# Kernel optimization log

Hardware: AMD Instinct MI355X
Metric: run time of the kernel (lower is better)

The kernel has to match this reference:

```python
import jax, jax.numpy as jnp
import numpy as np

B, S, HID = 2, 2048, 2048
H, HKV, D = 16, 4, 128        # num_heads, num_kv_heads, head_dim
G = H // HKV                   # GQA group size
CLIP = 8.0                     # clip_qkv
THETA = 10000.0                # rope_theta_within_seq
N_SEQS = 8                     # max_num_sequences


def setup_inputs() -> dict:
    key = jax.random.key(0)
    ks = jax.random.split(key, 6)
    hidden_states = jax.random.normal(ks[0], (B, S, HID), dtype=jnp.float32)
    within_seq_position_ids = jnp.broadcast_to(jnp.arange(S, dtype=jnp.int64), (B, S))
    global_position_ids = jnp.broadcast_to(jnp.arange(S, dtype=jnp.int64), (B, S))
    sequence_ids = jnp.sort(jax.random.randint(ks[1], (B, S), 0, N_SEQS, dtype=jnp.int64), axis=-1)
    scale = 0.02
    Wq = jax.random.normal(ks[2], (H * D, HID), dtype=jnp.float32) * scale
    Wk = jax.random.normal(ks[3], (HKV * D, HID), dtype=jnp.float32) * scale
    Wv = jax.random.normal(ks[4], (HKV * D, HID), dtype=jnp.float32) * scale
    Wo = jax.random.normal(ks[5], (HID, H * D), dtype=jnp.float32) * scale
    return {"hidden_states": hidden_states,
            "within_seq_position_ids": within_seq_position_ids,
            "global_position_ids": global_position_ids,
            "sequence_ids": sequence_ids,
            "Wq": Wq, "Wk": Wk, "Wv": Wv, "Wo": Wo}


def _rotate_half(x):
    x1, x2 = jnp.split(x, 2, axis=-1)
    return jnp.concatenate((-x2, x1), axis=-1)


def _rope_cos_sin(position_ids, dtype):
    # inv_freq: [D/2]
    inv_freq = THETA ** (-(jnp.arange(0, D, 2, dtype=jnp.float32) / D))
    angles = position_ids.astype(jnp.float32)[..., None] * inv_freq  # [B,S,D/2]
    angles = jnp.concatenate((angles, angles), axis=-1)              # [B,S,D]
    # unsqueeze head dim -> [B,S,1,D]
    return jnp.cos(angles)[:, :, None, :].astype(dtype), jnp.sin(angles)[:, :, None, :].astype(dtype)


def reference(hidden_states, within_seq_position_ids, global_position_ids, sequence_ids, Wq, Wk, Wv, Wo):
    b, s, _ = hidden_states.shape
    q = (hidden_states @ Wq.T).reshape(b, s, H, D)
    k = (hidden_states @ Wk.T).reshape(b, s, HKV, D)
    v = (hidden_states @ Wv.T).reshape(b, s, HKV, D)
    # clip_qkv
    q = jnp.clip(q, -CLIP, CLIP)
    k = jnp.clip(k, -CLIP, CLIP)
    v = jnp.clip(v, -CLIP, CLIP)
    # RoPE (within_seq layer -> within_seq_position_ids)
    cos, sin = _rope_cos_sin(within_seq_position_ids, q.dtype)
    q = q * cos + _rotate_half(q) * sin
    k = k * cos + _rotate_half(k) * sin
    # GQA: group queries by kv head instead of materializing repeat_kv
    q = q.transpose(0, 2, 1, 3).reshape(b, HKV, G, s, D)  # [B,HKV,G,S,D]
    k = k.transpose(0, 2, 1, 3)                            # [B,HKV,S,D]
    v = v.transpose(0, 2, 1, 3)
    scores = jnp.einsum('bhgqd,bhkd->bhgqk', q, k) / jnp.sqrt(jnp.asarray(D, q.dtype))
    # block-diagonal (same sequence) causal mask
    qi = jnp.arange(s)
    causal = qi[:, None] >= qi[None, :]                    # [S,S]
    same_seq = sequence_ids[:, :, None] == sequence_ids[:, None, :]  # [B,S,S]
    mask = (causal[None] & same_seq)[:, None, None, :, :]  # [B,1,1,S,S]
    scores = jnp.where(mask, scores, jnp.finfo(scores.dtype).min)
    attn = jax.nn.softmax(scores, axis=-1)
    out = jnp.einsum('bhgqk,bhkd->bhgqd', attn, v)         # [B,HKV,G,S,D]
    out = out.reshape(b, H, s, D).transpose(0, 2, 1, 3).reshape(b, s, H * D)
    return out @ Wo.T
```

## Files before the change

### kernel.cpp

```cpp
#include <hip/hip_runtime.h>
#include <hip/hip_bf16.h>

typedef __hip_bfloat16 bf16;
typedef __attribute__((ext_vector_type(8))) short bf16x8;
typedef __attribute__((ext_vector_type(4))) float f32x4;

#define MFMA_BF16(a, b, c) __builtin_amdgcn_mfma_f32_16x16x32_bf16((a), (b), (c), 0, 0, 0)

#define B_   2
#define S_   2048
#define HID_ 2048
#define H_   16
#define HKV_ 4
#define D_   128

#define GLOAD_LDS(gptr, lptr) \
  __builtin_amdgcn_global_load_lds((const __attribute__((address_space(1))) void*)(gptr), \
                                   (__attribute__((address_space(3))) void*)(lptr), 16, 0, 0)

template <int N>
__device__ __forceinline__ void vmw() {
  if constexpr (N == 0)      asm volatile("s_waitcnt vmcnt(0)" ::: "memory");
  else if constexpr (N == 3) asm volatile("s_waitcnt vmcnt(3)" ::: "memory");
  else                       asm volatile("s_waitcnt vmcnt(4)" ::: "memory");
}

__device__ __forceinline__ void blk_barrier() {
  __builtin_amdgcn_sched_barrier(0);
  __builtin_amdgcn_s_barrier();
  __builtin_amdgcn_sched_barrier(0);
}

__global__ void cvt_f32_bf16(const float* __restrict__ src, bf16* __restrict__ dst, int n) {
  int i = (blockIdx.x * 256 + threadIdx.x) * 4;
  if (i >= n) return;
  float4 v = *reinterpret_cast<const float4*>(src + i);
  alignas(8) bf16 t[4];
  t[0] = __float2bfloat16(v.x);
  t[1] = __float2bfloat16(v.y);
  t[2] = __float2bfloat16(v.z);
  t[3] = __float2bfloat16(v.w);
  *reinterpret_cast<short4*>(dst + i) = *reinterpret_cast<const short4*>(t);
}

__global__ void seq_start(const int* __restrict__ seq, int* __restrict__ sstart) {
  int t = blockIdx.x * 256 + threadIdx.x;
  int b = t >> 11, s = t & (S_ - 1);
  const int* sb = seq + b * S_;
  int sid = sb[s];
  int lo = 0, hi = s;
  while (lo < hi) {
    int mid = (lo + hi) >> 1;
    if (sb[mid] < sid) lo = mid + 1; else hi = mid;
  }
  sstart[t] = lo;
}

template <int BM, int OUT_BF16>
__global__ __launch_bounds__(512, 2) void gemm8p(const bf16* __restrict__ A,
                                                 const bf16* __restrict__ Bw,
                                                 void* __restrict__ Cout,
                                                 int M, int N, int K) {
  constexpr int BN = 256;
  constexpr int MR = BM / 32;
  constexpr int LA = BM / 128;
  constexpr int VCHK = (BM == 256) ? 4 : 3;

  __shared__ bf16 As[2][2][BM * 32];
  __shared__ bf16 Bs[2][2][BN * 32];

  const int tid  = threadIdx.x;
  const int lane = tid & 63;
  const int w    = tid >> 6;
  const int wr   = w >> 2;
  const int wc   = w & 3;
  const int ln15 = lane & 15, g = lane >> 4;

  const int nwg = gridDim.x;
  int bid = blockIdx.x;
  bid = (bid & 7) * (nwg >> 3) + (bid >> 3);
  const int nbn = N / BN;
  const int m0 = (bid / nbn) * BM;
  const int n0 = (bid % nbn) * BN;

  f32x4 acc[MR][4] = {};

  auto stageA = [&](int db, int kh, int t) {
    int kc = t * 64 + kh * 32;
#pragma unroll
    for (int r = 0; r < LA; r++) {
      int sIdx = r * 512 + tid;
      int row = sIdx >> 2;
      int ss = (sIdx & 3) ^ ((row >> 1) & 3);
      GLOAD_LDS(A + (size_t)(m0 + row) * K + kc + ss * 8, &As[db][kh][(r * 512 + w * 64) * 8]);
    }
  };
  auto stageB = [&](int db, int kh, int t) {
    int kc = t * 64 + kh * 32;
#pragma unroll
    for (int r = 0; r < 2; r++) {
      int sIdx = r * 512 + tid;
      int row = sIdx >> 2;
      int ss = (sIdx & 3) ^ ((row >> 1) & 3);
      GLOAD_LDS(Bw + (size_t)(n0 + row) * K + kc + ss * 8, &Bs[db][kh][(r * 512 + w * 64) * 8]);
    }
  };
  auto rdA = [&](bf16x8 (&af)[4], int db, int kh, int mb) {
#pragma unroll
    for (int m = 0; m < 4; m++) {
      int row = wr * (BM / 2) + (mb + m) * 16 + ln15;
      af[m] = *reinterpret_cast<const bf16x8*>(&As[db][kh][row * 32 + ((g ^ ((row >> 1) & 3)) << 3)]);
    }
  };
  auto rdB = [&](bf16x8 (&bfr)[4], int db, int kh) {
#pragma unroll
    for (int n = 0; n < 4; n++) {
      int row = wc * 64 + n * 16 + ln15;
      bfr[n] = *reinterpret_cast<const bf16x8*>(&Bs[db][kh][row * 32 + ((g ^ ((row >> 1) & 3)) << 3)]);
    }
  };

  bf16x8 af[4], bfr[4];
  auto MF = [&](int mb) {
    __builtin_amdgcn_s_setprio(1);
#pragma unroll
    for (int m = 0; m < 4; m++)
#pragma unroll
      for (int n = 0; n < 4; n++)
        acc[mb + m][n] = MFMA_BF16(af[m], bfr[n], acc[mb + m][n]);
    __builtin_amdgcn_s_setprio(0);
  };

  const int NT = K >> 6;

  stageA(0, 0, 0); stageB(0, 0, 0);
  stageA(0, 1, 0); stageB(0, 1, 0);
  stageA(1, 0, 1); stageB(1, 0, 1);
  vmw<VCHK>();
  blk_barrier();

  for (int T = 0; T < NT; ++T) {
    const int db = T & 1, dn = db ^ 1;
    const bool tail = (T >= NT - 3);

    if constexpr (BM == 256) {
      rdA(af, db, 0, 0); rdB(bfr, db, 0);
      if (T + 1 < NT) stageA(dn, 1, T + 1);
      blk_barrier(); MF(0); blk_barrier();
      rdA(af, db, 0, 4);
      if (T + 1 < NT) stageB(dn, 1, T + 1);
      if (tail) vmw<0>(); else vmw<4>();
      blk_barrier(); MF(4); blk_barrier();
      rdA(af, db, 1, 0); rdB(bfr, db, 1);
      if (T + 2 < NT) stageA(db, 0, T + 2);
      blk_barrier(); MF(0); blk_barrier();
      rdA(af, db, 1, 4);
      if (T + 2 < NT) stageB(db, 0, T + 2);
      if (tail) vmw<0>(); else vmw<4>();
      blk_barrier(); MF(4); blk_barrier();
    } else {
      rdA(af, db, 0, 0); rdB(bfr, db, 0);
      if (T + 1 < NT) { stageA(dn, 1, T + 1); stageB(dn, 1, T + 1); }
      if (tail) vmw<0>(); else vmw<3>();
      blk_barrier(); MF(0); blk_barrier();
      rdA(af, db, 1, 0); rdB(bfr, db, 1);
      if (T + 2 < NT) { stageA(db, 0, T + 2); stageB(db, 0, T + 2); }
      if (tail) vmw<0>(); else vmw<3>();
      blk_barrier(); MF(0); blk_barrier();
    }
  }

#pragma unroll
  for (int m = 0; m < MR; m++)
#pragma unroll
    for (int n = 0; n < 4; n++)
#pragma unroll
      for (int r = 0; r < 4; r++) {
        int row = m0 + wr * (BM / 2) + m * 16 + g * 4 + r;
        int col = n0 + wc * 64 + n * 16 + ln15;
        if constexpr (OUT_BF16) {
          ((bf16*)Cout)[(size_t)row * N + col] = __float2bfloat16(acc[m][n][r]);
        } else {
          ((float*)Cout)[(size_t)row * N + col] = acc[m][n][r];
        }
      }
}

__global__ __launch_bounds__(256) void qkv_post(const bf16* __restrict__ QKV,
                                                const int* __restrict__ wpos,
                                                bf16* __restrict__ Qs,
                                                bf16* __restrict__ Ks,
                                                bf16* __restrict__ Vt) {
  const int row = blockIdx.x;
  const int b = row >> 11, s = row & (S_ - 1);
  const int t = threadIdx.x;
  const bf16* R = QKV + (size_t)row * 3072;
  const float pos = (float)wpos[row];
  const float kln = 0.14391156831212787f;
  const float qscale = 0.08838834764831845f;

  for (int p = t; p < 1024; p += 256) {
    int h = p >> 6, i = p & 63;
    float ang = pos * expf(-(float)i * kln);
    float sn, cs;
    sincosf(ang, &sn, &cs);
    float x1 = __bfloat162float(R[h * 128 + i]);
    float x2 = __bfloat162float(R[h * 128 + 64 + i]);
    x1 = fminf(fmaxf(x1, -8.f), 8.f);
    x2 = fminf(fmaxf(x2, -8.f), 8.f);
    float y1 = (x1 * cs - x2 * sn) * qscale;
    float y2 = (x2 * cs + x1 * sn) * qscale;
    size_t qb = ((size_t)(b * H_ + h) * S_ + s) * D_;
    Qs[qb + i]      = __float2bfloat16(y1);
    Qs[qb + 64 + i] = __float2bfloat16(y2);
  }
  {
    int kh = t >> 6, i = t & 63;
    float ang = pos * expf(-(float)i * kln);
    float sn, cs;
    sincosf(ang, &sn, &cs);
    float x1 = __bfloat162float(R[2048 + kh * 128 + i]);
    float x2 = __bfloat162float(R[2048 + kh * 128 + 64 + i]);
    x1 = fminf(fmaxf(x1, -8.f), 8.f);
    x2 = fminf(fmaxf(x2, -8.f), 8.f);
    float y1 = x1 * cs - x2 * sn;
    float y2 = x2 * cs + x1 * sn;
    size_t kb = ((size_t)(b * HKV_ + kh) * S_ + s) * D_;
    Ks[kb + i]      = __float2bfloat16(y1);
    Ks[kb + 64 + i] = __float2bfloat16(y2);
  }
  for (int e = t; e < 512; e += 256) {
    int kh = e >> 7, d = e & 127;
    float x = __bfloat162float(R[2560 + e]);
    x = fminf(fmaxf(x, -8.f), 8.f);
    Vt[((size_t)(b * HKV_ + kh) * D_ + d) * S_ + s] = __float2bfloat16(x);
  }
}

__global__ __launch_bounds__(256) void attn_fwd(const bf16* __restrict__ Qs,
                                                const bf16* __restrict__ Ks,
                                                const bf16* __restrict__ Vt,
                                                const int* __restrict__ sstart,
                                                bf16* __restrict__ att) {
  __shared__ bf16 Kl[2][32 * 128];
  __shared__ bf16 Vl[2][128 * 32];
  __shared__ bf16 Plds[4][16 * 32];

  const int tid = threadIdx.x;
  const int lane = tid & 63, w = tid >> 6;
  const int ln15 = lane & 15, g = lane >> 4;

  const int wg = ((blockIdx.x & 7) << 7) | (blockIdx.x >> 3);
  const int qt  = wg & 127;
  const int kvh = (wg >> 7) & 3;
  const int b   = wg >> 9;
  const int h   = kvh * 4 + w;
  const int q0  = qt * 16;
  const int qi  = q0 + ln15;

  const bf16* Qrow = Qs + ((size_t)(b * H_ + h) * S_ + qi) * D_;
  bf16x8 qf[4];
#pragma unroll
  for (int c = 0; c < 4; c++)
    qf[c] = *reinterpret_cast<const bf16x8*>(Qrow + c * 32 + g * 8);

  const int sQ = sstart[b * S_ + qi];
  const int kstart = __builtin_amdgcn_readfirstlane(__shfl(sQ, 0));
  const int kend = q0 + 15;

  const bf16* Kb = Ks + (size_t)(b * HKV_ + kvh) * S_ * D_;
  const bf16* Vb = Vt + (size_t)(b * HKV_ + kvh) * D_ * S_;

  auto stage = [&](int buf, int kb) {
#pragma unroll
    for (int p = 0; p < 2; p++) {
      int slot = p * 256 + tid;
      int row = slot >> 4;
      int cs = (slot & 15) ^ (row & 15);
      int gr = min(kb + row, S_ - 1);
      GLOAD_LDS(Kb + (size_t)gr * D_ + cs * 8, &Kl[buf][(p * 256 + w * 64) * 8]);
    }
#pragma unroll
    for (int p = 0; p < 2; p++) {
      int slot = p * 256 + tid;
      int d = slot >> 2, c = slot & 3;
      int cs = c ^ (d & 3);
      int gcol = min(kb + cs * 8, S_ - 8);
      GLOAD_LDS(Vb + (size_t)d * S_ + gcol, &Vl[buf][(p * 256 + w * 64) * 8]);
    }
  };

  float m = -1e30f, lsum = 0.f;
  f32x4 o[8] = {};

  stage(0, kstart);
  int buf = 0;
  for (int kb = kstart; kb <= kend; kb += 32) {
    __syncthreads();
    if (kb + 32 <= kend) stage(buf ^ 1, kb + 32);

    bf16x8 kf0[4], kf1[4];
#pragma unroll
    for (int c = 0; c < 4; c++) {
      kf0[c] = *reinterpret_cast<const bf16x8*>(&Kl[buf][ln15 * 128 + (((c * 4 + g) ^ ln15) << 3)]);
      kf1[c] = *reinterpret_cast<const bf16x8*>(&Kl[buf][(16 + ln15) * 128 + (((c * 4 + g) ^ ln15) << 3)]);
    }
    f32x4 s0 = {0.f, 0.f, 0.f, 0.f}, s1 = {0.f, 0.f, 0.f, 0.f};
#pragma unroll
    for (int c = 0; c < 4; c++) {
      s0 = MFMA_BF16(kf0[c], qf[c], s0);
      s1 = MFMA_BF16(kf1[c], qf[c], s1);
    }

    float sc[8];
    float tmax = -1e30f;
#pragma unroll
    for (int r = 0; r < 4; r++) {
      int k0i = kb + g * 4 + r;
      int k1i = k0i + 16;
      float x0 = (k0i >= sQ && k0i <= qi) ? s0[r] : -1e30f;
      float x1 = (k1i >= sQ && k1i <= qi) ? s1[r] : -1e30f;
      sc[r] = x0;
      sc[4 + r] = x1;
      tmax = fmaxf(tmax, fmaxf(x0, x1));
    }
    tmax = fmaxf(tmax, __shfl_xor(tmax, 16));
    tmax = fmaxf(tmax, __shfl_xor(tmax, 32));
    float mn  = fmaxf(m, tmax);
    float fac = __expf(m - mn);
    float ps = 0.f;
    alignas(16) bf16 pb[8];
#pragma unroll
    for (int i2 = 0; i2 < 8; i2++) {
      float p = (sc[i2] < -1e29f) ? 0.f : __expf(sc[i2] - mn);
      ps += p;
      pb[i2] = __float2bfloat16(p);
    }
    ps += __shfl_xor(ps, 16);
    ps += __shfl_xor(ps, 32);
    lsum = lsum * fac + ps;
    m = mn;
#pragma unroll
    for (int t2 = 0; t2 < 8; t2++) o[t2] *= fac;

    *reinterpret_cast<short4*>(&Plds[w][ln15 * 32 + g * 4])      = *reinterpret_cast<const short4*>(&pb[0]);
    *reinterpret_cast<short4*>(&Plds[w][ln15 * 32 + 16 + g * 4]) = *reinterpret_cast<const short4*>(&pb[4]);
    __builtin_amdgcn_wave_barrier();
    bf16x8 pf = *reinterpret_cast<const bf16x8*>(&Plds[w][ln15 * 32 + g * 8]);

#pragma unroll
    for (int t2 = 0; t2 < 8; t2++) {
      int d = t2 * 16 + ln15;
      bf16x8 vf = *reinterpret_cast<const bf16x8*>(&Vl[buf][d * 32 + ((g ^ (ln15 & 3)) << 3)]);
      o[t2] = MFMA_BF16(vf, pf, o[t2]);
    }
    __builtin_amdgcn_wave_barrier();
    buf ^= 1;
  }

  float inv = 1.f / lsum;
#pragma unroll
  for (int t2 = 0; t2 < 8; t2++)
#pragma unroll
    for (int r = 0; r < 4; r++) {
      int d = t2 * 16 + g * 4 + r;
      att[((size_t)(b * S_ + qi)) * (H_ * D_) + h * D_ + d] = __float2bfloat16(o[t2][r] * inv);
    }
}

extern "C" void kernel_launch(void* const* d_in, const int* in_sizes, int n_in,
                              void* d_out, int out_size, void* d_ws, size_t ws_size,
                              hipStream_t stream) {
  const float* hidden = (const float*)d_in[0];
  const int* wpos = (const int*)d_in[1];
  const int* seq = (const int*)d_in[3];
  const float* Wq = (const float*)d_in[4];
  const float* Wk = (const float*)d_in[5];
  const float* Wv = (const float*)d_in[6];
  const float* Wo = (const float*)d_in[7];

  char* ws = (char*)d_ws;
  bf16* Xb   = (bf16*)(ws);
  bf16* Wqkv = (bf16*)(ws + 16777216);
  bf16* Wob  = (bf16*)(ws + 29360128);
  bf16* QKVb = (bf16*)(ws + 37748736);
  bf16* Ksb  = (bf16*)(ws + 62914560);
  bf16* Vtb  = (bf16*)(ws + 67108864);
  int*  sst  = (int*)(ws + 71303168);
  bf16* Qsb  = Xb;
  bf16* attb = QKVb;

  cvt_f32_bf16<<<dim3(8192), dim3(256), 0, stream>>>(hidden, Xb, 8388608);
  cvt_f32_bf16<<<dim3(4096), dim3(256), 0, stream>>>(Wq, Wqkv, 4194304);
  cvt_f32_bf16<<<dim3(1024), dim3(256), 0, stream>>>(Wk, Wqkv + 4194304, 1048576);
  cvt_f32_bf16<<<dim3(1024), dim3(256), 0, stream>>>(Wv, Wqkv + 5242880, 1048576);
  cvt_f32_bf16<<<dim3(4096), dim3(256), 0, stream>>>(Wo, Wob, 4194304);
  seq_start<<<dim3(32), dim3(256), 0, stream>>>(seq, sst);

  gemm8p<256, 1><<<dim3(192), dim3(512), 0, stream>>>(Xb, Wqkv, (void*)QKVb, 4096, 3072, 2048);

  qkv_post<<<dim3(4096), dim3(256), 0, stream>>>(QKVb, wpos, Qsb, Ksb, Vtb);

  attn_fwd<<<dim3(1024), dim3(256), 0, stream>>>(Qsb, Ksb, Vtb, sst, attb);

  gemm8p<128, 0><<<dim3(256), dim3(512), 0, stream>>>(attb, Wob, d_out, 4096, 2048, 2048);
}
```

Before: 187.8 us.

## Retile both GEMMs to fill 256 CUs and merge weight conversion kernels

The GEMM kernel is generalised over BN. The QKV projection now uses 256x192 tiles and the output projection uses 256x128 tiles, so both launch 256 workgroups instead of 192 or uneven shapes, which better matches the CU count. The B-tile staging and the vmcnt wait schedule are restructured for the new tile widths. The four weight conversion launches are merged into one kernel to cut launch overhead. Risks are a lower arithmetic intensity per tile with narrower BN and a more intricate wait-count pipeline.

```diff
diff --git a/kernel.cpp b/kernel.cpp
--- a/kernel.cpp
+++ b/kernel.cpp
@@ -21,8 +21,11 @@
 template <int N>
 __device__ __forceinline__ void vmw() {
   if constexpr (N == 0)      asm volatile("s_waitcnt vmcnt(0)" ::: "memory");
+  else if constexpr (N == 2) asm volatile("s_waitcnt vmcnt(2)" ::: "memory");
   else if constexpr (N == 3) asm volatile("s_waitcnt vmcnt(3)" ::: "memory");
-  else                       asm volatile("s_waitcnt vmcnt(4)" ::: "memory");
+  else if constexpr (N == 4) asm volatile("s_waitcnt vmcnt(4)" ::: "memory");
+  else if constexpr (N == 5) asm volatile("s_waitcnt vmcnt(5)" ::: "memory");
+  else                       asm volatile("s_waitcnt vmcnt(6)" ::: "memory");
 }
 
 __device__ __forceinline__ void blk_barrier() {
@@ -43,6 +46,24 @@
   *reinterpret_cast<short4*>(dst + i) = *reinterpret_cast<const short4*>(t);
 }
 
+__global__ void cvt_weights(const float* __restrict__ Wq, const float* __restrict__ Wk,
+                            const float* __restrict__ Wv, const float* __restrict__ Wo,
+                            bf16* __restrict__ Wqkv, bf16* __restrict__ Wob) {
+  int i = (blockIdx.x * 256 + threadIdx.x) * 4;
+  const float* src; bf16* dst; int off;
+  if (i < 4194304)      { src = Wq; dst = Wqkv;           off = i; }
+  else if (i < 5242880) { src = Wk; dst = Wqkv + 4194304; off = i - 4194304; }
+  else if (i < 6291456) { src = Wv; dst = Wqkv + 5242880; off = i - 5242880; }
+  else                  { src = Wo; dst = Wob;            off = i - 6291456; }
+  float4 v = *reinterpret_cast<const float4*>(src + off);
+  alignas(8) bf16 t[4];
+  t[0] = __float2bfloat16(v.x);
+  t[1] = __float2bfloat16(v.y);
+  t[2] = __float2bfloat16(v.z);
+  t[3] = __float2bfloat16(v.w);
+  *reinterpret_cast<short4*>(dst + off) = *reinterpret_cast<const short4*>(t);
+}
+
 __global__ void seq_start(const int* __restrict__ seq, int* __restrict__ sstart) {
   int t = blockIdx.x * 256 + threadIdx.x;
   int b = t >> 11, s = t & (S_ - 1);
@@ -56,15 +77,14 @@
   sstart[t] = lo;
 }
 
-template <int BM, int OUT_BF16>
+template <int BM, int BN, int OUT_BF16>
 __global__ __launch_bounds__(512, 2) void gemm8p(const bf16* __restrict__ A,
                                                  const bf16* __restrict__ Bw,
                                                  void* __restrict__ Cout,
                                                  int M, int N, int K) {
-  constexpr int BN = 256;
   constexpr int MR = BM / 32;
+  constexpr int NR = BN / 64;
   constexpr int LA = BM / 128;
-  constexpr int VCHK = (BM == 256) ? 4 : 3;
 
   __shared__ bf16 As[2][2][BM * 32];
   __shared__ bf16 Bs[2][2][BN * 32];
@@ -83,7 +103,7 @@
   const int m0 = (bid / nbn) * BM;
   const int n0 = (bid % nbn) * BN;
 
-  f32x4 acc[MR][4] = {};
+  f32x4 acc[MR][NR] = {};
 
   auto stageA = [&](int db, int kh, int t) {
     int kc = t * 64 + kh * 32;
@@ -95,89 +115,105 @@
       GLOAD_LDS(A + (size_t)(m0 + row) * K + kc + ss * 8, &As[db][kh][(r * 512 + w * 64) * 8]);
     }
   };
-  auto stageB = [&](int db, int kh, int t) {
-    int kc = t * 64 + kh * 32;
-#pragma unroll
-    for (int r = 0; r < 2; r++) {
-      int sIdx = r * 512 + tid;
-      int row = sIdx >> 2;
-      int ss = (sIdx & 3) ^ ((row >> 1) & 3);
-      GLOAD_LDS(Bw + (size_t)(n0 + row) * K + kc + ss * 8, &Bs[db][kh][(r * 512 + w * 64) * 8]);
-    }
-  };
-  auto rdA = [&](bf16x8 (&af)[4], int db, int kh, int mb) {
+  auto stageB_r = [&](int db, int t, int r) {
+    int slot = r * 512 + tid;
+    int frow = slot >> 2;
+    int kh = frow >= BN;
+    int brow = frow - kh * BN;
+    int ss = (slot & 3) ^ ((brow >> 1) & 3);
+    GLOAD_LDS(Bw + (size_t)(n0 + brow) * K + t * 64 + kh * 32 + ss * 8,
+              &Bs[db][0][0] + (size_t)(r * 512 + w * 64) * 8);
+  };
+  auto stageB_h = [&](int db, int kh, int t) {
+    int brow = tid >> 2;
+    int ss = (tid & 3) ^ ((brow >> 1) & 3);
+    GLOAD_LDS(Bw + (size_t)(n0 + brow) * K + t * 64 + kh * 32 + ss * 8,
+              &Bs[db][kh][(w * 64) * 8]);
+  };
+
+  bf16x8 af[4], bfr[NR];
+  auto rdA = [&](int db, int kh, int mb) {
 #pragma unroll
     for (int m = 0; m < 4; m++) {
       int row = wr * (BM / 2) + (mb + m) * 16 + ln15;
       af[m] = *reinterpret_cast<const bf16x8*>(&As[db][kh][row * 32 + ((g ^ ((row >> 1) & 3)) << 3)]);
     }
   };
-  auto rdB = [&](bf16x8 (&bfr)[4], int db, int kh) {
-#pragma unroll
-    for (int n = 0; n < 4; n++) {
-      int row = wc * 64 + n * 16 + ln15;
+  auto rdB = [&](int db, int kh) {
+#pragma unroll
+    for (int n = 0; n < NR; n++) {
+      int row = wc * (BN / 4) + n * 16 + ln15;
       bfr[n] = *reinterpret_cast<const bf16x8*>(&Bs[db][kh][row * 32 + ((g ^ ((row >> 1) & 3)) << 3)]);
     }
   };
-
-  bf16x8 af[4], bfr[4];
   auto MF = [&](int mb) {
     __builtin_amdgcn_s_setprio(1);
 #pragma unroll
     for (int m = 0; m < 4; m++)
 #pragma unroll
-      for (int n = 0; n < 4; n++)
+      for (int n = 0; n < NR; n++)
         acc[mb + m][n] = MFMA_BF16(af[m], bfr[n], acc[mb + m][n]);
     __builtin_amdgcn_s_setprio(0);
   };
 
   const int NT = K >> 6;
 
-  stageA(0, 0, 0); stageB(0, 0, 0);
-  stageA(0, 1, 0); stageB(0, 1, 0);
-  stageA(1, 0, 1); stageB(1, 0, 1);
-  vmw<VCHK>();
+  if constexpr (BN == 192) {
+    stageA(0, 0, 0);
+    stageB_r(0, 0, 0); stageB_r(0, 0, 1);
+    stageA(0, 1, 0);
+    stageB_r(0, 0, 2);
+    stageA(1, 0, 1);
+    vmw<5>();
+  } else {
+    stageA(0, 0, 0);
+    stageB_h(0, 0, 0);
+    stageA(0, 1, 0);
+    stageB_h(0, 1, 0);
+    stageA(1, 0, 1);
+    stageB_h(1, 0, 1);
+    vmw<6>();
+  }
   blk_barrier();
 
   for (int T = 0; T < NT; ++T) {
     const int db = T & 1, dn = db ^ 1;
-    const bool tail = (T >= NT - 3);
-
-    if constexpr (BM == 256) {
-      rdA(af, db, 0, 0); rdB(bfr, db, 0);
-      if (T + 1 < NT) stageA(dn, 1, T + 1);
-      blk_barrier(); MF(0); blk_barrier();
-      rdA(af, db, 0, 4);
-      if (T + 1 < NT) stageB(dn, 1, T + 1);
+    const bool tail = (T >= NT - 2);
+
+    rdA(db, 0, 0); rdB(db, 0);
+    if (T + 1 < NT) stageA(dn, 1, T + 1);
+    blk_barrier(); MF(0); blk_barrier();
+    rdA(db, 0, 4);
+    if constexpr (BN == 192) {
+      if (T + 1 < NT) { stageB_r(dn, T + 1, 0); stageB_r(dn, T + 1, 1); }
       if (tail) vmw<0>(); else vmw<4>();
-      blk_barrier(); MF(4); blk_barrier();
-      rdA(af, db, 1, 0); rdB(bfr, db, 1);
-      if (T + 2 < NT) stageA(db, 0, T + 2);
-      blk_barrier(); MF(0); blk_barrier();
-      rdA(af, db, 1, 4);
-      if (T + 2 < NT) stageB(db, 0, T + 2);
-      if (tail) vmw<0>(); else vmw<4>();
-      blk_barrier(); MF(4); blk_barrier();
     } else {
-      rdA(af, db, 0, 0); rdB(bfr, db, 0);
-      if (T + 1 < NT) { stageA(dn, 1, T + 1); stageB(dn, 1, T + 1); }
+      if (T + 1 < NT) stageB_h(dn, 1, T + 1);
+      if (tail) vmw<0>(); else vmw<6>();
+    }
+    blk_barrier(); MF(4); blk_barrier();
+    rdA(db, 1, 0); rdB(db, 1);
+    if (T + 2 < NT) stageA(db, 0, T + 2);
+    blk_barrier(); MF(0); blk_barrier();
+    rdA(db, 1, 4);
+    if constexpr (BN == 192) {
+      if (T + 1 < NT) stageB_r(dn, T + 1, 2);
       if (tail) vmw<0>(); else vmw<3>();
-      blk_barrier(); MF(0); blk_barrier();
-      rdA(af, db, 1, 0); rdB(bfr, db, 1);
-      if (T + 2 < NT) { stageA(db, 0, T + 2); stageB(db, 0, T + 2); }
-      if (tail) vmw<0>(); else vmw<3>();
-      blk_barrier(); MF(0); blk_barrier();
-    }
+    } else {
+      if (T + 2 < NT) stageB_h(db, 0, T + 2);
+      if (tail) vmw<0>(); else vmw<6>();
+    }
+    blk_barrier(); MF(4); blk_barrier();
   }
 
 #pragma unroll
   for (int m = 0; m < MR; m++)
 #pragma unroll
-    for (int n = 0; n < 4; n++)
+    for (int n = 0; n < NR; n++)
 #pragma unroll
       for (int r = 0; r < 4; r++) {
         int row = m0 + wr * (BM / 2) + m * 16 + g * 4 + r;
-        int col = n0 + wc * 64 + n * 16 + ln15;
+        int col = n0 + wc * (BN / 4) + n * 16 + ln15;
         if constexpr (OUT_BF16) {
           ((bf16*)Cout)[(size_t)row * N + col] = __float2bfloat16(acc[m][n][r]);
         } else {
@@ -391,17 +427,14 @@
   bf16* attb = QKVb;
 
   cvt_f32_bf16<<<dim3(8192), dim3(256), 0, stream>>>(hidden, Xb, 8388608);
-  cvt_f32_bf16<<<dim3(4096), dim3(256), 0, stream>>>(Wq, Wqkv, 4194304);
-  cvt_f32_bf16<<<dim3(1024), dim3(256), 0, stream>>>(Wk, Wqkv + 4194304, 1048576);
-  cvt_f32_bf16<<<dim3(1024), dim3(256), 0, stream>>>(Wv, Wqkv + 5242880, 1048576);
-  cvt_f32_bf16<<<dim3(4096), dim3(256), 0, stream>>>(Wo, Wob, 4194304);
+  cvt_weights<<<dim3(10240), dim3(256), 0, stream>>>(Wq, Wk, Wv, Wo, Wqkv, Wob);
   seq_start<<<dim3(32), dim3(256), 0, stream>>>(seq, sst);
 
-  gemm8p<256, 1><<<dim3(192), dim3(512), 0, stream>>>(Xb, Wqkv, (void*)QKVb, 4096, 3072, 2048);
+  gemm8p<256, 192, 1><<<dim3(256), dim3(512), 0, stream>>>(Xb, Wqkv, (void*)QKVb, 4096, 3072, 2048);
 
   qkv_post<<<dim3(4096), dim3(256), 0, stream>>>(QKVb, wpos, Qsb, Ksb, Vtb);
 
   attn_fwd<<<dim3(1024), dim3(256), 0, stream>>>(Qsb, Ksb, Vtb, sst, attb);
 
-  gemm8p<128, 0><<<dim3(256), dim3(512), 0, stream>>>(attb, Wob, d_out, 4096, 2048, 2048);
-}
+  gemm8p<256, 128, 0><<<dim3(256), dim3(512), 0, stream>>>(attb, Wob, d_out, 4096, 2048, 2048);
+}
```

After: 179.2 us. -4.6%, faster.
